# Kernel tuning notes

Measured on AMD Instinct MI355X. Metric: run time of the kernel, lower is better.

## Reference

```python
import jax, jax.numpy as jnp
import numpy as np

B, D, S, SE, H, DFF = 4, 1024, 1024, 1024, 16, 4096
DH = D // H
NUDGE = 1e-7


def norm(x):
    # x: [B, D, S]; custom layer norm: mean over (1,2), then divide by full L2 norm
    size = x.shape[1] * x.shape[2]
    mean = jnp.sum(x, axis=(1, 2)) / size
    x = x - mean[:, None, None]
    std = jnp.sqrt(jnp.sum(x * x, axis=(1, 2)))
    return x / (std[:, None, None] + NUDGE)


def mha(q_in, kv_in, Wq, Wk, Wv, Wo, causal):
    # q_in: [B, Sq, D], kv_in: [B, Sk, D]
    Bq, Sq, _ = q_in.shape
    Sk = kv_in.shape[1]
    q = (q_in @ Wq).reshape(Bq, Sq, H, DH)
    k = (kv_in @ Wk).reshape(Bq, Sk, H, DH)
    v = (kv_in @ Wv).reshape(Bq, Sk, H, DH)
    scores = jnp.einsum('bqhd,bkhd->bhqk', q, k) / jnp.sqrt(jnp.asarray(DH, q.dtype))
    if causal:
        mask = jnp.tril(jnp.ones((Sq, Sk), dtype=bool))
        scores = jnp.where(mask, scores, jnp.finfo(scores.dtype).min)
    attn = jax.nn.softmax(scores, axis=-1)
    out = jnp.einsum('bhqk,bkhd->bqhd', attn, v).reshape(Bq, Sq, D)
    return out @ Wo


def setup_inputs() -> dict:
    key = jax.random.key(0)
    ks = jax.random.split(key, 13)
    w = lambda k, sh: jax.random.normal(k, sh, dtype=jnp.float32) * 0.02
    return {
        'embedding': jax.random.normal(ks[0], (B, D, SE), dtype=jnp.float32),
        'other_inputs': jax.random.normal(ks[1], (B, D, S), dtype=jnp.float32),
        'Wq_s': w(ks[2], (D, D)), 'Wk_s': w(ks[3], (D, D)),
        'Wv_s': w(ks[4], (D, D)), 'Wo_s': w(ks[5], (D, D)),
        'Wq_c': w(ks[6], (D, D)), 'Wk_c': w(ks[7], (D, D)),
        'Wv_c': w(ks[8], (D, D)), 'Wo_c': w(ks[9], (D, D)),
        'W1': w(ks[10], (D, DFF)), 'b1': jnp.zeros((DFF,), jnp.float32),
        'W2': w(ks[11], (DFF, D)), 'b2': jnp.zeros((D,), jnp.float32),
    }


def reference(embedding, other_inputs, Wq_s, Wk_s, Wv_s, Wo_s,
              Wq_c, Wk_c, Wv_c, Wo_c, W1, b1, W2, b2):
    # tensors are [B, D, S]; attention operates on [B, S, D]
    x = other_inputs.transpose(0, 2, 1)
    sa = mha(x, x, Wq_s, Wk_s, Wv_s, Wo_s, causal=True)
    post_attention = norm(other_inputs + sa.transpose(0, 2, 1))

    pa = post_attention.transpose(0, 2, 1)
    emb = embedding.transpose(0, 2, 1)
    ca = mha(pa, emb, Wq_c, Wk_c, Wv_c, Wo_c, causal=False)
    post_embedding = norm(post_attention + ca.transpose(0, 2, 1))

    # per-token MLP (original loops over axis 2 and restacks; here fully batched)
    pe = post_embedding.transpose(0, 2, 1)  # [B, S, D]
    ff = jax.nn.relu(pe @ W1 + b1) @ W2 + b2
    return norm(post_embedding + ff.transpose(0, 2, 1))
```

## Files before the change

kernel.cpp:

```cpp
#include <hip/hip_runtime.h>
#include <cmath>

#define B_   4
#define D_   1024
#define S_   1024
#define H_   16
#define DH_  64
#define DFF_ 4096

typedef __attribute__((ext_vector_type(8))) short bf16x8;
typedef __attribute__((ext_vector_type(4))) float f32x4;

__device__ __forceinline__ unsigned short f2b(float f) {
    unsigned int u = __float_as_uint(f);
    u += 0x7fffu + ((u >> 16) & 1u);
    return (unsigned short)(u >> 16);
}

__device__ __forceinline__ void gload_lds16(const unsigned short* g, unsigned short* l) {
    __builtin_amdgcn_global_load_lds(
        (const __attribute__((address_space(1))) void*)g,
        (__attribute__((address_space(3))) void*)l, 16, 0, 0);
}

template <int BM, int BN, bool RES>
__global__ __launch_bounds__(256, 2)
void gemm_t(const unsigned short* __restrict__ A,
            const unsigned short* __restrict__ Wt,
            const float* __restrict__ bias,
            const float* __restrict__ residual,
            float* __restrict__ Cf, unsigned short* __restrict__ Cb,
            float* __restrict__ partial,
            int N, int K, int lda, int ldb, long csplit, int relu)
{
    constexpr int FM = BM / 32, FN = BN / 32;
    __shared__ unsigned short As[BM * 32];
    __shared__ unsigned short Bs[BN * 32];
    const int tid = threadIdx.x;
    const int w = tid >> 6, lane = tid & 63;
    const int quad = lane >> 4, l16 = lane & 15;
    const int m0 = blockIdx.y * BM, n0 = blockIdx.x * BN;
    const int wm = (w >> 1) * (BM / 2), wn = (w & 1) * (BN / 2);
    const int srow = lane >> 2, scol = (lane & 3) * 8;

    A  += (size_t)blockIdx.z * K;
    Wt += (size_t)blockIdx.z * K;
    if (Cf) Cf += (size_t)blockIdx.z * csplit;

    f32x4 acc[FM][FN] = {};

    for (int k0 = 0; k0 < K; k0 += 32) {
#pragma unroll
        for (int i = 0; i < BM / 64; ++i)
            gload_lds16(A + (size_t)(m0 + (w + 4 * i) * 16 + srow) * lda + k0 + scol,
                        As + (w + 4 * i) * 512);
#pragma unroll
        for (int i = 0; i < BN / 64; ++i)
            gload_lds16(Wt + (size_t)(n0 + (w + 4 * i) * 16 + srow) * ldb + k0 + scol,
                        Bs + (w + 4 * i) * 512);
        __syncthreads();

        bf16x8 af[FM], bfr[FN];
#pragma unroll
        for (int i = 0; i < FM; ++i)
            af[i] = *(const bf16x8*)&As[(wm + i * 16 + l16) * 32 + quad * 8];
#pragma unroll
        for (int j = 0; j < FN; ++j)
            bfr[j] = *(const bf16x8*)&Bs[(wn + j * 16 + l16) * 32 + quad * 8];
#pragma unroll
        for (int i = 0; i < FM; ++i)
#pragma unroll
            for (int j = 0; j < FN; ++j)
                acc[i][j] = __builtin_amdgcn_mfma_f32_16x16x32_bf16(af[i], bfr[j], acc[i][j], 0, 0, 0);
        __syncthreads();
    }

    float s = 0.f, ss = 0.f;
#pragma unroll
    for (int i = 0; i < FM; ++i) {
        const int grow = m0 + wm + i * 16 + quad * 4;
#pragma unroll
        for (int j = 0; j < FN; ++j) {
            const int gcol = n0 + wn + j * 16 + l16;
            const float bv = bias ? bias[gcol] : 0.f;
#pragma unroll
            for (int r = 0; r < 4; ++r) {
                float vv = acc[i][j][r] + bv;
                if (relu) vv = fmaxf(vv, 0.f);
                if constexpr (RES) {
                    vv += residual[(size_t)(grow + r) * N + gcol];
                    s += vv; ss += vv * vv;
                    Cf[(size_t)(grow + r) * N + gcol] = vv;
                } else {
                    if (Cf) Cf[(size_t)(grow + r) * N + gcol] = vv;
                    if (Cb) Cb[(size_t)(grow + r) * N + gcol] = f2b(vv);
                }
            }
        }
    }

    if constexpr (RES) {
        float* rs = (float*)As;
        float* rss = rs + 256;
        rs[tid] = s; rss[tid] = ss;
        __syncthreads();
        for (int off = 128; off > 0; off >>= 1) {
            if (tid < off) { rs[tid] += rs[tid + off]; rss[tid] += rss[tid + off]; }
            __syncthreads();
        }
        if (tid == 0) {
            constexpr int YPB = S_ / BM;
            const int b = blockIdx.y / YPB;
            const int chunk = (blockIdx.y % YPB) * gridDim.x + blockIdx.x;
            const int chunks = YPB * gridDim.x;
            partial[((size_t)b * chunks + chunk) * 2 + 0] = rs[0];
            partial[((size_t)b * chunks + chunk) * 2 + 1] = rss[0];
        }
    }
}

__global__ void reduce4_res(const float* __restrict__ pc, const float* __restrict__ res,
                            const float* __restrict__ bias, float* __restrict__ y,
                            float* __restrict__ partial)
{
    const size_t pcs = (size_t)4096 * 1024;
    const int b = blockIdx.y;
    const size_t base = (size_t)b * 1048576 + (size_t)blockIdx.x * 16384;
    float s = 0.f, ss = 0.f;
    for (int i = threadIdx.x; i < 4096; i += 256) {
        const size_t e = base + (size_t)i * 4;
        float4 v0 = *(const float4*)&pc[e];
        float4 v1 = *(const float4*)&pc[e + pcs];
        float4 v2 = *(const float4*)&pc[e + 2 * pcs];
        float4 v3 = *(const float4*)&pc[e + 3 * pcs];
        float4 rv = *(const float4*)&res[e];
        float4 bv = *(const float4*)&bias[e & 1023];
        float4 o;
        o.x = v0.x + v1.x + v2.x + v3.x + rv.x + bv.x;
        o.y = v0.y + v1.y + v2.y + v3.y + rv.y + bv.y;
        o.z = v0.z + v1.z + v2.z + v3.z + rv.z + bv.z;
        o.w = v0.w + v1.w + v2.w + v3.w + rv.w + bv.w;
        *(float4*)&y[e] = o;
        s += o.x + o.y + o.z + o.w;
        ss += o.x * o.x + o.y * o.y + o.z * o.z + o.w * o.w;
    }
    __shared__ float rs[256], rss[256];
    rs[threadIdx.x] = s; rss[threadIdx.x] = ss;
    __syncthreads();
    for (int off = 128; off > 0; off >>= 1) {
        if (threadIdx.x < off) {
            rs[threadIdx.x] += rs[threadIdx.x + off];
            rss[threadIdx.x] += rss[threadIdx.x + off];
        }
        __syncthreads();
    }
    if (threadIdx.x == 0) {
        partial[((size_t)b * 64 + blockIdx.x) * 2 + 0] = rs[0];
        partial[((size_t)b * 64 + blockIdx.x) * 2 + 1] = rss[0];
    }
}

__device__ __forceinline__ void stats_reduce(const float* __restrict__ partial,
                                             int b, int chunks, int tid,
                                             float* rs, float* rss,
                                             float& mean, float& inv)
{
    float s = 0.f, ss = 0.f;
    for (int i = tid; i < chunks; i += 256) {
        s  += partial[((size_t)b * chunks + i) * 2 + 0];
        ss += partial[((size_t)b * chunks + i) * 2 + 1];
    }
    rs[tid] = s; rss[tid] = ss;
    __syncthreads();
    for (int off = 128; off > 0; off >>= 1) {
        if (tid < off) { rs[tid] += rs[tid + off]; rss[tid] += rss[tid + off]; }
        __syncthreads();
    }
    const float size = (float)(D_ * S_);
    const float m = rs[0] / size;
    const float var = fmaxf(rss[0] - size * m * m, 0.f);
    mean = m;
    inv = 1.f / (sqrtf(var) + 1e-7f);
    __syncthreads();
}

__global__ void norm_apply_dual(float* __restrict__ y, unsigned short* __restrict__ yb,
                                const float* __restrict__ partial, int chunks)
{
    __shared__ float rs[256], rss[256];
    const int b = blockIdx.y;
    float mean, inv;
    stats_reduce(partial, b, chunks, threadIdx.x, rs, rss, mean, inv);

    const int perBatch = D_ * S_;
    float4* y4 = (float4*)(y + (size_t)b * perBatch);
    unsigned short* yb_ = yb + (size_t)b * perBatch;
    const int n4 = perBatch / 4;
    for (int i = blockIdx.x * blockDim.x + threadIdx.x; i < n4;
         i += gridDim.x * blockDim.x) {
        float4 v = y4[i];
        v.x = (v.x - mean) * inv; v.y = (v.y - mean) * inv;
        v.z = (v.z - mean) * inv; v.w = (v.w - mean) * inv;
        y4[i] = v;
        ushort4 hh; hh.x = f2b(v.x); hh.y = f2b(v.y); hh.z = f2b(v.z); hh.w = f2b(v.w);
        *(ushort4*)(yb_ + (size_t)i * 4) = hh;
    }
}

template <bool CAUSAL>
__global__ __launch_bounds__(256, 2)
void attn_mfma2(const unsigned short* __restrict__ q, const unsigned short* __restrict__ k,
                const unsigned short* __restrict__ vt, unsigned short* __restrict__ o,
                int qstride, int kstride)
{
    __shared__ unsigned short Ks[64][72];
    __shared__ unsigned short Vt[64][72];
    __shared__ unsigned short Ps[4][2][16][72];
    const int tid = threadIdx.x;
    const int w = tid >> 6, lane = tid & 63;
    const int quad = lane >> 4, l16 = lane & 15;
    const int h = blockIdx.y, b = blockIdx.z;
    const int bx = blockIdx.x, q0 = bx * 128;

    const unsigned short* qA = q + (size_t)(b * S_ + q0 + w * 16 + l16) * qstride + h * DH_;
    const unsigned short* qB = qA + (size_t)64 * qstride;
    const bf16x8 qa0 = *(const bf16x8*)(qA + quad * 8);
    const bf16x8 qa1 = *(const bf16x8*)(qA + 32 + quad * 8);
    const bf16x8 qb0 = *(const bf16x8*)(qB + quad * 8);
    const bf16x8 qb1 = *(const bf16x8*)(qB + 32 + quad * 8);

    f32x4 OA[4] = {}, OB[4] = {};
    float lA[4] = {}, lB[4] = {};

    const int nblk = CAUSAL ? (2 * bx + 2) : (S_ / 64);
    for (int t = 0; t < nblk; ++t) {
        const int j0 = t * 64;
#pragma unroll
        for (int it = 0; it < 2; ++it) {
            const int id2 = tid + it * 256;
            const int row = id2 >> 3, c8 = (id2 & 7) * 8;
            *(bf16x8*)&Ks[row][c8] =
                *(const bf16x8*)(k + (size_t)(b * S_ + j0 + row) * kstride + h * DH_ + c8);
            *(bf16x8*)&Vt[row][c8] =
                *(const bf16x8*)(vt + (size_t)((b * H_ + h) * DH_ + row) * S_ + j0 + c8);
        }
        __syncthreads();

        const bool doA = !CAUSAL || (t <= 2 * bx);
        const bool diagA = CAUSAL && (t == 2 * bx);
        const bool diagB = CAUSAL && (t == 2 * bx + 1);

        f32x4 stA[4], stB[4];
#pragma unroll
        for (int n = 0; n < 4; ++n) {
            const bf16x8 kf0 = *(const bf16x8*)&Ks[n * 16 + l16][quad * 8];
            const bf16x8 kf1 = *(const bf16x8*)&Ks[n * 16 + l16][32 + quad * 8];
            if (doA) {
                f32x4 c = {};
                c = __builtin_amdgcn_mfma_f32_16x16x32_bf16(qa0, kf0, c, 0, 0, 0);
                c = __builtin_amdgcn_mfma_f32_16x16x32_bf16(qa1, kf1, c, 0, 0, 0);
                stA[n] = c;
            }
            f32x4 c = {};
            c = __builtin_amdgcn_mfma_f32_16x16x32_bf16(qb0, kf0, c, 0, 0, 0);
            c = __builtin_amdgcn_mfma_f32_16x16x32_bf16(qb1, kf1, c, 0, 0, 0);
            stB[n] = c;
        }

        if (doA) {
#pragma unroll
            for (int n = 0; n < 4; ++n)
#pragma unroll
                for (int r = 0; r < 4; ++r) {
                    float sv = stA[n][r] * 0.125f;
                    if (diagA) {
                        const int row = q0 + w * 16 + quad * 4 + r;
                        const int key = j0 + n * 16 + l16;
                        if (key > row) sv = -1e30f;
                    }
                    const float p = __expf(sv);
                    lA[r] += p;
                    Ps[w][0][quad * 4 + r][n * 16 + l16] = f2b(p);
                }
        }
#pragma unroll
        for (int n = 0; n < 4; ++n)
#pragma unroll
            for (int r = 0; r < 4; ++r) {
                float sv = stB[n][r] * 0.125f;
                if (diagB) {
                    const int row = q0 + 64 + w * 16 + quad * 4 + r;
                    const int key = j0 + n * 16 + l16;
                    if (key > row) sv = -1e30f;
                }
                const float p = __expf(sv);
                lB[r] += p;
                Ps[w][1][quad * 4 + r][n * 16 + l16] = f2b(p);
            }
        __threadfence_block();

        const bf16x8 pa0 = *(const bf16x8*)&Ps[w][0][l16][quad * 8];
        const bf16x8 pa1 = *(const bf16x8*)&Ps[w][0][l16][32 + quad * 8];
        const bf16x8 pb0 = *(const bf16x8*)&Ps[w][1][l16][quad * 8];
        const bf16x8 pb1 = *(const bf16x8*)&Ps[w][1][l16][32 + quad * 8];
#pragma unroll
        for (int n = 0; n < 4; ++n) {
            const bf16x8 vf0 = *(const bf16x8*)&Vt[n * 16 + l16][quad * 8];
            const bf16x8 vf1 = *(const bf16x8*)&Vt[n * 16 + l16][32 + quad * 8];
            if (doA) {
                OA[n] = __builtin_amdgcn_mfma_f32_16x16x32_bf16(pa0, vf0, OA[n], 0, 0, 0);
                OA[n] = __builtin_amdgcn_mfma_f32_16x16x32_bf16(pa1, vf1, OA[n], 0, 0, 0);
            }
            OB[n] = __builtin_amdgcn_mfma_f32_16x16x32_bf16(pb0, vf0, OB[n], 0, 0, 0);
            OB[n] = __builtin_amdgcn_mfma_f32_16x16x32_bf16(pb1, vf1, OB[n], 0, 0, 0);
        }
        __syncthreads();
    }

#pragma unroll
    for (int r = 0; r < 4; ++r) {
        float la = lA[r], lb = lB[r];
        la += __shfl_xor(la, 1); la += __shfl_xor(la, 2);
        la += __shfl_xor(la, 4); la += __shfl_xor(la, 8);
        lb += __shfl_xor(lb, 1); lb += __shfl_xor(lb, 2);
        lb += __shfl_xor(lb, 4); lb += __shfl_xor(lb, 8);
        const float ia = 1.f / la, ib = 1.f / lb;
        const size_t baseA = (size_t)(b * S_ + q0 + w * 16 + quad * 4 + r) * D_ + h * DH_;
        const size_t baseB = baseA + (size_t)64 * D_;
#pragma unroll
        for (int n = 0; n < 4; ++n) {
            o[baseA + n * 16 + l16] = f2b(OA[n][r] * ia);
            o[baseB + n * 16 + l16] = f2b(OB[n][r] * ib);
        }
    }
}

__global__ void transpose_v(const unsigned short* __restrict__ src,
                            unsigned short* __restrict__ dst, int istride)
{
    __shared__ unsigned short t[32][34];
    const int z = blockIdx.z, b = z >> 4, h = z & 15;
    const int s0 = blockIdx.x * 32, d0 = blockIdx.y * 32;
    const int tx = threadIdx.x, ty = threadIdx.y;
#pragma unroll
    for (int i = 0; i < 4; ++i)
        t[ty + i * 8][tx] =
            src[(size_t)(b * S_ + s0 + ty + i * 8) * istride + h * DH_ + d0 + tx];
    __syncthreads();
#pragma unroll
    for (int i = 0; i < 4; ++i)
        dst[(size_t)(z * DH_ + d0 + ty + i * 8) * S_ + s0 + tx] = t[tx][ty + i * 8];
}

struct SrcPack { const float* p[8]; };

__global__ void wtrans8(SrcPack pk, unsigned short* __restrict__ dst)
{
    __shared__ float tile[32][33];
    const int z = blockIdx.z;
    const float* src = pk.p[z];
    const int c0 = blockIdx.x * 32, r0 = blockIdx.y * 32;
    const int tx = threadIdx.x, ty = threadIdx.y;
#pragma unroll
    for (int i = 0; i < 4; ++i)
        tile[ty + i * 8][tx] = src[(size_t)(r0 + ty + i * 8) * 1024 + c0 + tx];
    __syncthreads();
#pragma unroll
    for (int i = 0; i < 4; ++i)
        dst[(size_t)z * 1048576 + (size_t)(c0 + ty + i * 8) * 1024 + r0 + tx] =
            f2b(tile[tx][ty + i * 8]);
}

__global__ void transpose_dual(const float* __restrict__ in, float* __restrict__ outf,
                               unsigned short* __restrict__ outb, int R, int C,
                               const float* __restrict__ partial, int chunks)
{
    __shared__ float tile[32][33];
    __shared__ float rs[256], rss[256];
    const int z = blockIdx.z;
    const int tx = threadIdx.x, ty = threadIdx.y;
    const int tid = ty * 32 + tx;

    float mean = 0.f, inv = 1.f;
    if (partial) {
        float s = 0.f, ss = 0.f;
        for (int i = tid; i < chunks; i += 256) {
            s  += partial[((size_t)z * chunks + i) * 2 + 0];
            ss += partial[((size_t)z * chunks + i) * 2 + 1];
        }
        rs[tid] = s; rss[tid] = ss;
        __syncthreads();
        for (int off = 128; off > 0; off >>= 1) {
            if (tid < off) { rs[tid] += rs[tid + off]; rss[tid] += rss[tid + off]; }
            __syncthreads();
        }
        const float size = (float)(D_ * S_);
        mean = rs[0] / size;
        const float var = fmaxf(rss[0] - size * mean * mean, 0.f);
        inv = 1.f / (sqrtf(var) + 1e-7f);
        __syncthreads();
    }

    const float* ip = in + (size_t)z * R * C;
    const int c0 = blockIdx.x * 32, r0 = blockIdx.y * 32;
#pragma unroll
    for (int i = 0; i < 4; ++i)
        tile[ty + i * 8][tx] = ip[(size_t)(r0 + ty + i * 8) * C + c0 + tx];
    __syncthreads();
#pragma unroll
    for (int i = 0; i < 4; ++i) {
        const float v = (tile[tx][ty + i * 8] - mean) * inv;
        const size_t oidx = (size_t)z * R * C + (size_t)(c0 + ty + i * 8) * R + r0 + tx;
        if (outf) outf[oidx] = v;
        if (outb) outb[oidx] = f2b(v);
    }
}

extern "C" void kernel_launch(void* const* d_in, const int* in_sizes, int n_in,
                              void* d_out, int out_size, void* d_ws, size_t ws_size,
                              hipStream_t stream)
{
    const float* embedding = (const float*)d_in[0];
    const float* other     = (const float*)d_in[1];
    const float* W1 = (const float*)d_in[10];
    const float* b1 = (const float*)d_in[11];
    const float* W2 = (const float*)d_in[12];
    const float* b2 = (const float*)d_in[13];
    float* out = (float*)d_out;

    char* wsb = (char*)d_ws;
    const size_t MB = 1u << 20;
    float* f0 = (float*)(wsb + 0 * MB);
    float* f2 = (float*)(wsb + 16 * MB);
    unsigned short* wts  = (unsigned short*)(wsb + 32 * MB);
    unsigned short* wqkv = wts;
    unsigned short* wo_s = wts + 3 * 1048576;
    unsigned short* wq_c = wts + 4 * 1048576;
    unsigned short* wkv_c= wts + 5 * 1048576;
    unsigned short* wo_c = wts + 7 * 1048576;
    unsigned short* w1t  = wts + 8 * 1048576;
    unsigned short* w2t  = wts + 12 * 1048576;
    unsigned short* actA = (unsigned short*)(wsb + 64 * MB);
    unsigned short* actB = (unsigned short*)(wsb + 72 * MB);
    unsigned short* actC = (unsigned short*)(wsb + 80 * MB);
    unsigned short* actC2 = actC + 4 * 1048576;
    float* pc      = (float*)(wsb + 112 * MB);
    float* partial = (float*)(wsb + 176 * MB);

    const dim3 blkT(32, 8), blk256(256);
    const dim3 gT(32, 32, B_);
    const dim3 gAttn(S_ / 128, H_, B_);
    const dim3 gVt(32, 2, B_ * H_);
    const dim3 gApply(64, B_);

    SrcPack pk;
    pk.p[0] = (const float*)d_in[2]; pk.p[1] = (const float*)d_in[3];
    pk.p[2] = (const float*)d_in[4]; pk.p[3] = (const float*)d_in[5];
    pk.p[4] = (const float*)d_in[6]; pk.p[5] = (const float*)d_in[7];
    pk.p[6] = (const float*)d_in[8]; pk.p[7] = (const float*)d_in[9];
    hipLaunchKernelGGL(wtrans8, dim3(32, 32, 8), blkT, 0, stream, pk, wts);
    hipLaunchKernelGGL(transpose_dual, dim3(128, 32, 1), blkT, 0, stream, W1, nullptr, w1t, 1024, 4096, nullptr, 0);
    hipLaunchKernelGGL(transpose_dual, dim3(32, 128, 1), blkT, 0, stream, W2, nullptr, w2t, 4096, 1024, nullptr, 0);

    hipLaunchKernelGGL(transpose_dual, gT, blkT, 0, stream, other, f0, actA, D_, S_, nullptr, 0);

    hipLaunchKernelGGL((gemm_t<128, 128, false>), dim3(24, 32), blk256, 0, stream,
                       actA, wqkv, nullptr, nullptr, nullptr, actC, nullptr,
                       3072, 1024, 1024, 1024, 0L, 0);
    hipLaunchKernelGGL(transpose_v, gVt, blkT, 0, stream, actC + 2048, actA, 3072);
    hipLaunchKernelGGL(attn_mfma2<true>, gAttn, blk256, 0, stream,
                       actC, actC + 1024, actA, actB, 3072, 3072);
    hipLaunchKernelGGL((gemm_t<64, 128, true>), dim3(8, 64), blk256, 0, stream,
                       actB, wo_s, nullptr, f0, f2, nullptr, partial,
                       1024, 1024, 1024, 1024, 0L, 0);
    hipLaunchKernelGGL(norm_apply_dual, gApply, blk256, 0, stream, f2, actA, partial, 128);

    hipLaunchKernelGGL(transpose_dual, gT, blkT, 0, stream, embedding, nullptr, actB, D_, S_, nullptr, 0);
    hipLaunchKernelGGL((gemm_t<64, 128, false>), dim3(8, 64), blk256, 0, stream,
                       actA, wq_c, nullptr, nullptr, nullptr, actC, nullptr,
                       1024, 1024, 1024, 1024, 0L, 0);
    hipLaunchKernelGGL((gemm_t<128, 128, false>), dim3(16, 32), blk256, 0, stream,
                       actB, wkv_c, nullptr, nullptr, nullptr, actC2, nullptr,
                       2048, 1024, 1024, 1024, 0L, 0);
    hipLaunchKernelGGL(transpose_v, gVt, blkT, 0, stream, actC2 + 1024, actB, 2048);
    hipLaunchKernelGGL(attn_mfma2<false>, gAttn, blk256, 0, stream,
                       actC, actC2, actB, actA, 1024, 2048);
    hipLaunchKernelGGL((gemm_t<64, 128, true>), dim3(8, 64), blk256, 0, stream,
                       actA, wo_c, nullptr, f2, f0, nullptr, partial,
                       1024, 1024, 1024, 1024, 0L, 0);
    hipLaunchKernelGGL(norm_apply_dual, gApply, blk256, 0, stream, f0, actA, partial, 128);

    hipLaunchKernelGGL((gemm_t<128, 128, false>), dim3(32, 32), blk256, 0, stream,
                       actA, w1t, b1, nullptr, nullptr, actC, nullptr,
                       DFF_, 1024, 1024, 1024, 0L, 1);
    hipLaunchKernelGGL((gemm_t<128, 128, false>), dim3(8, 32, 4), blk256, 0, stream,
                       actC, w2t, nullptr, nullptr, pc, nullptr, nullptr,
                       1024, 1024, 4096, 4096, (long)4096 * 1024, 0);
    hipLaunchKernelGGL(reduce4_res, gApply, blk256, 0, stream, pc, f0, b2, f2, partial);
    hipLaunchKernelGGL(transpose_dual, gT, blkT, 0, stream, f2, out, nullptr, S_, D_, partial, 64);

    (void)in_sizes; (void)n_in; (void)out_size; (void)ws_size;
}
```

Baseline: 547.6 us.

## Swap GEMM grid axes, rotate causal tiles per head, halve FFN2 split-K

Swaps the GEMM grid so blockIdx.x walks M tiles and blockIdx.y walks N tiles. Consecutive blocks then share the same weight tile, which should improve L2 reuse. In causal attention the query tile index is rotated by the head index, so each dispatch wave mixes long and short rows and the load is more even. The FFN down-projection split-K drops from 4 to 2, halving the partial-sum traffic in the reduce kernel at the cost of fewer blocks per launch (512 instead of 1024).

```diff
diff --git a/kernel.cpp b/kernel.cpp
--- a/kernel.cpp
+++ b/kernel.cpp
@@ -39,7 +39,7 @@
     const int tid = threadIdx.x;
     const int w = tid >> 6, lane = tid & 63;
     const int quad = lane >> 4, l16 = lane & 15;
-    const int m0 = blockIdx.y * BM, n0 = blockIdx.x * BN;
+    const int m0 = blockIdx.x * BM, n0 = blockIdx.y * BN;
     const int wm = (w >> 1) * (BM / 2), wn = (w & 1) * (BN / 2);
     const int srow = lane >> 2, scol = (lane & 3) * 8;
 
@@ -110,16 +110,16 @@
         }
         if (tid == 0) {
             constexpr int YPB = S_ / BM;
-            const int b = blockIdx.y / YPB;
-            const int chunk = (blockIdx.y % YPB) * gridDim.x + blockIdx.x;
-            const int chunks = YPB * gridDim.x;
+            const int b = blockIdx.x / YPB;
+            const int chunk = (blockIdx.x % YPB) * gridDim.y + blockIdx.y;
+            const int chunks = YPB * gridDim.y;
             partial[((size_t)b * chunks + chunk) * 2 + 0] = rs[0];
             partial[((size_t)b * chunks + chunk) * 2 + 1] = rss[0];
         }
     }
 }
 
-__global__ void reduce4_res(const float* __restrict__ pc, const float* __restrict__ res,
+__global__ void reduce2_res(const float* __restrict__ pc, const float* __restrict__ res,
                             const float* __restrict__ bias, float* __restrict__ y,
                             float* __restrict__ partial)
 {
@@ -131,15 +131,13 @@
         const size_t e = base + (size_t)i * 4;
         float4 v0 = *(const float4*)&pc[e];
         float4 v1 = *(const float4*)&pc[e + pcs];
-        float4 v2 = *(const float4*)&pc[e + 2 * pcs];
-        float4 v3 = *(const float4*)&pc[e + 3 * pcs];
         float4 rv = *(const float4*)&res[e];
         float4 bv = *(const float4*)&bias[e & 1023];
         float4 o;
-        o.x = v0.x + v1.x + v2.x + v3.x + rv.x + bv.x;
-        o.y = v0.y + v1.y + v2.y + v3.y + rv.y + bv.y;
-        o.z = v0.z + v1.z + v2.z + v3.z + rv.z + bv.z;
-        o.w = v0.w + v1.w + v2.w + v3.w + rv.w + bv.w;
+        o.x = v0.x + v1.x + rv.x + bv.x;
+        o.y = v0.y + v1.y + rv.y + bv.y;
+        o.z = v0.z + v1.z + rv.z + bv.z;
+        o.w = v0.w + v1.w + rv.w + bv.w;
         *(float4*)&y[e] = o;
         s += o.x + o.y + o.z + o.w;
         ss += o.x * o.x + o.y * o.y + o.z * o.z + o.w * o.w;
@@ -220,7 +218,8 @@
     const int w = tid >> 6, lane = tid & 63;
     const int quad = lane >> 4, l16 = lane & 15;
     const int h = blockIdx.y, b = blockIdx.z;
-    const int bx = blockIdx.x, q0 = bx * 128;
+    const int qt = CAUSAL ? ((blockIdx.x + h) & 7) : blockIdx.x;
+    const int q0 = qt * 128;
 
     const unsigned short* qA = q + (size_t)(b * S_ + q0 + w * 16 + l16) * qstride + h * DH_;
     const unsigned short* qB = qA + (size_t)64 * qstride;
@@ -232,7 +231,7 @@
     f32x4 OA[4] = {}, OB[4] = {};
     float lA[4] = {}, lB[4] = {};
 
-    const int nblk = CAUSAL ? (2 * bx + 2) : (S_ / 64);
+    const int nblk = CAUSAL ? (2 * qt + 2) : (S_ / 64);
     for (int t = 0; t < nblk; ++t) {
         const int j0 = t * 64;
 #pragma unroll
@@ -246,9 +245,9 @@
         }
         __syncthreads();
 
-        const bool doA = !CAUSAL || (t <= 2 * bx);
-        const bool diagA = CAUSAL && (t == 2 * bx);
-        const bool diagB = CAUSAL && (t == 2 * bx + 1);
+        const bool doA = !CAUSAL || (t <= 2 * qt);
+        const bool diagA = CAUSAL && (t == 2 * qt);
+        const bool diagB = CAUSAL && (t == 2 * qt + 1);
 
         f32x4 stA[4], stB[4];
 #pragma unroll
@@ -464,28 +463,28 @@
 
     hipLaunchKernelGGL(transpose_dual, gT, blkT, 0, stream, other, f0, actA, D_, S_, nullptr, 0);
 
-    hipLaunchKernelGGL((gemm_t<128, 128, false>), dim3(24, 32), blk256, 0, stream,
+    hipLaunchKernelGGL((gemm_t<128, 128, false>), dim3(32, 24), blk256, 0, stream,
                        actA, wqkv, nullptr, nullptr, nullptr, actC, nullptr,
                        3072, 1024, 1024, 1024, 0L, 0);
     hipLaunchKernelGGL(transpose_v, gVt, blkT, 0, stream, actC + 2048, actA, 3072);
     hipLaunchKernelGGL(attn_mfma2<true>, gAttn, blk256, 0, stream,
                        actC, actC + 1024, actA, actB, 3072, 3072);
-    hipLaunchKernelGGL((gemm_t<64, 128, true>), dim3(8, 64), blk256, 0, stream,
+    hipLaunchKernelGGL((gemm_t<64, 128, true>), dim3(64, 8), blk256, 0, stream,
                        actB, wo_s, nullptr, f0, f2, nullptr, partial,
                        1024, 1024, 1024, 1024, 0L, 0);
     hipLaunchKernelGGL(norm_apply_dual, gApply, blk256, 0, stream, f2, actA, partial, 128);
 
     hipLaunchKernelGGL(transpose_dual, gT, blkT, 0, stream, embedding, nullptr, actB, D_, S_, nullptr, 0);
-    hipLaunchKernelGGL((gemm_t<64, 128, false>), dim3(8, 64), blk256, 0, stream,
+    hipLaunchKernelGGL((gemm_t<64, 128, false>), dim3(64, 8), blk256, 0, stream,
                        actA, wq_c, nullptr, nullptr, nullptr, actC, nullptr,
                        1024, 1024, 1024, 1024, 0L, 0);
-    hipLaunchKernelGGL((gemm_t<128, 128, false>), dim3(16, 32), blk256, 0, stream,
+    hipLaunchKernelGGL((gemm_t<128, 128, false>), dim3(32, 16), blk256, 0, stream,
                        actB, wkv_c, nullptr, nullptr, nullptr, actC2, nullptr,
                        2048, 1024, 1024, 1024, 0L, 0);
     hipLaunchKernelGGL(transpose_v, gVt, blkT, 0, stream, actC2 + 1024, actB, 2048);
     hipLaunchKernelGGL(attn_mfma2<false>, gAttn, blk256, 0, stream,
                        actC, actC2, actB, actA, 1024, 2048);
-    hipLaunchKernelGGL((gemm_t<64, 128, true>), dim3(8, 64), blk256, 0, stream,
+    hipLaunchKernelGGL((gemm_t<64, 128, true>), dim3(64, 8), blk256, 0, stream,
                        actA, wo_c, nullptr, f2, f0, nullptr, partial,
                        1024, 1024, 1024, 1024, 0L, 0);
     hipLaunchKernelGGL(norm_apply_dual, gApply, blk256, 0, stream, f0, actA, partial, 128);
@@ -493,10 +492,10 @@
     hipLaunchKernelGGL((gemm_t<128, 128, false>), dim3(32, 32), blk256, 0, stream,
                        actA, w1t, b1, nullptr, nullptr, actC, nullptr,
                        DFF_, 1024, 1024, 1024, 0L, 1);
-    hipLaunchKernelGGL((gemm_t<128, 128, false>), dim3(8, 32, 4), blk256, 0, stream,
+    hipLaunchKernelGGL((gemm_t<128, 128, false>), dim3(32, 8, 2), blk256, 0, stream,
                        actC, w2t, nullptr, nullptr, pc, nullptr, nullptr,
-                       1024, 1024, 4096, 4096, (long)4096 * 1024, 0);
-    hipLaunchKernelGGL(reduce4_res, gApply, blk256, 0, stream, pc, f0, b2, f2, partial);
+                       1024, 2048, 4096, 4096, (long)4096 * 1024, 0);
+    hipLaunchKernelGGL(reduce2_res, gApply, blk256, 0, stream, pc, f0, b2, f2, partial);
     hipLaunchKernelGGL(transpose_dual, gT, blkT, 0, stream, f2, out, nullptr, S_, D_, partial, 64);
 
     (void)in_sizes; (void)n_in; (void)out_size; (void)ws_size;
```

Measured after the change: 535.0 us. 2.3% less time.
